# Optimization experiments

Measured on AMD Instinct MI355X. Metric: run time of the kernel, lower is better.

Reference implementation:

```python
import jax, jax.numpy as jnp
import numpy as np

NEG_BIG = 1e30  # matches the 1e+30 masking constant in the original


def setup_inputs() -> dict:
    key = jax.random.key(0)
    ks = jax.random.split(key, 6)
    B, Lc, Lq, D = 8, 512, 64, 256
    return {
        "context": jax.random.normal(ks[0], (B, Lc, D), jnp.float32),
        "question": jax.random.normal(ks[1], (B, Lq, D), jnp.float32),
        "mask": jnp.ones((B, Lq), jnp.int32),
        "att_w": jax.random.normal(ks[2], (3 * D,), jnp.float32) * 0.05,  # Linear(6H=3D -> 1) weight
        "att_b": jnp.zeros((1,), jnp.float32),                            # Linear bias
        "w_in": jax.random.normal(ks[3], (D,), jnp.float32) * 0.05,       # input_linear (no bias)
        "w_mem": jax.random.normal(ks[4], (D,), jnp.float32) * 0.05,      # memory_linear (no bias)
    }


def reference(context, question, mask, att_w, att_b, w_in, w_mem):
    # context: [B,Lc,D], question: [B,Lq,D], mask: [B,Lq] (0/1)
    D = context.shape[-1]
    # Separable (mathematically identical) form of Linear(cat([c, q, c*q])):
    # score[b,i,j] = c_i . w_c + q_j . w_q + sum_d c[b,i,d]*q[b,j,d]*w_p[d] + b
    w_c, w_q, w_p = att_w[:D], att_w[D:2 * D], att_w[2 * D:]
    sc = jnp.einsum('bid,d->bi', context, w_c)                 # [B,Lc]
    sq = jnp.einsum('bjd,d->bj', question, w_q)                # [B,Lq]
    sp = jnp.einsum('bid,bjd->bij', context * w_p, question)   # [B,Lc,Lq]
    attention = sc[:, :, None] + sq[:, None, :] + sp + att_b[0]

    maskf = mask.astype(attention.dtype)
    masked = attention - NEG_BIG * (1.0 - maskf)[:, None, :]   # [B,Lc,Lq]

    ctx1 = jnp.einsum('bid,d->bi', context, w_in)[..., None]   # input_linear:  [B,Lc,1]
    q1 = jnp.einsum('bjd,d->bj', question, w_mem)[..., None]   # memory_linear: [B,Lq,1]

    h_aware_weight = jax.nn.softmax(masked, axis=-1)           # [B,Lc,Lq]
    U = jnp.matmul(h_aware_weight, q1)                         # [B,Lc,1]

    u_aware_weight = jax.nn.softmax(jnp.max(masked, axis=-1), axis=-1)[:, None, :]  # [B,1,Lc]
    H = jnp.matmul(u_aware_weight, ctx1)                       # [B,1,1]

    G = jnp.concatenate([ctx1, U, ctx1 * U, U * H], axis=-1)   # [B,Lc,4]
    return G
```

## Files before the change

kernel.cpp:

```cpp
#include <hip/hip_runtime.h>

#define NB 8
#define LC 512
#define LQ 64
#define DD 256
#define NEG_BIG_F 1e30f

#define TPB 512
#define NWAVE 8
#define RPB 8
#define BPB (LC / RPB)

__device__ __forceinline__ float bcastf(float x, int lane) {
  return __uint_as_float((unsigned)__builtin_amdgcn_readlane((int)__float_as_uint(x), lane));
}

__global__ __launch_bounds__(TPB, 4) void rows_kernel(
    const float* __restrict__ context,
    const float* __restrict__ question,
    const int*   __restrict__ mask,
    const float* __restrict__ att_w,
    const float* __restrict__ att_b,
    const float* __restrict__ w_in,
    const float* __restrict__ w_mem,
    float4* __restrict__ ws4)
{
  __shared__ float4 T[64][64];
  __shared__ float sq_raw[LQ];
  __shared__ float q1_s[LQ];

  const int tid  = threadIdx.x;
  const int w    = tid >> 6;
  const int l    = tid & 63;
  const int b    = blockIdx.x / BPB;
  const int row0 = (blockIdx.x % BPB) * RPB;
  const int i    = row0 + w;

  const float4 wc4 = ((const float4*)att_w)[l];
  const float4 wq4 = ((const float4*)(att_w + DD))[l];
  const float4 wp4 = ((const float4*)(att_w + 2 * DD))[l];
  const float4 wi4 = ((const float4*)w_in)[l];
  const float4 wm4 = ((const float4*)w_mem)[l];
  const float4 c4  = ((const float4*)(context + ((size_t)b * LC + i) * DD))[l];

  float4 v[8];
#pragma unroll
  for (int k = 0; k < 8; ++k)
    v[k] = ((const float4*)(question + ((size_t)b * LQ + (k * 8 + w)) * DD))[l];
#pragma unroll
  for (int k = 0; k < 8; ++k)
    T[l][(k * 8 + w) ^ (l & 7)] = v[k];

  float psq[8], pq1[8];
#pragma unroll
  for (int k = 0; k < 8; ++k) {
    psq[k] = v[k].x*wq4.x + v[k].y*wq4.y + v[k].z*wq4.z + v[k].w*wq4.w;
    pq1[k] = v[k].x*wm4.x + v[k].y*wm4.y + v[k].z*wm4.z + v[k].w*wm4.w;
  }
#pragma unroll
  for (int off = 32; off > 0; off >>= 1) {
#pragma unroll
    for (int k = 0; k < 8; ++k) {
      psq[k] += __shfl_xor(psq[k], off);
      pq1[k] += __shfl_xor(pq1[k], off);
    }
  }
  if (l == 0) {
#pragma unroll
    for (int k = 0; k < 8; ++k) {
      sq_raw[k * 8 + w] = psq[k];
      q1_s[k * 8 + w]   = pq1[k];
    }
  }

  float4 cp;
  cp.x = c4.x*wp4.x; cp.y = c4.y*wp4.y; cp.z = c4.z*wp4.z; cp.w = c4.w*wp4.w;
  float sc = c4.x*wc4.x + c4.y*wc4.y + c4.z*wc4.z + c4.w*wc4.w;
  float c1 = c4.x*wi4.x + c4.y*wi4.y + c4.z*wi4.z + c4.w*wi4.w;
#pragma unroll
  for (int off = 32; off > 0; off >>= 1) {
    sc += __shfl_xor(sc, off);
    c1 += __shfl_xor(c1, off);
  }

  __syncthreads();

  float a0 = 0.f, a1 = 0.f, a2 = 0.f, a3 = 0.f;
#pragma unroll
  for (int c = 0; c < 64; ++c) {
    float4 qv = T[c][l ^ (c & 7)];
    a0 += bcastf(cp.x, c) * qv.x;
    a1 += bcastf(cp.y, c) * qv.y;
    a2 += bcastf(cp.z, c) * qv.z;
    a3 += bcastf(cp.w, c) * qv.w;
  }

  const float mf = (float)mask[b * LQ + l];
  const float vscore = (a0 + a1) + (a2 + a3) + sc + sq_raw[l] + att_b[0]
                       - NEG_BIG_F * (1.0f - mf);
  const float q1_l = q1_s[l];

  float m = vscore;
#pragma unroll
  for (int off = 32; off > 0; off >>= 1) m = fmaxf(m, __shfl_xor(m, off));
  float p  = __expf(vscore - m);
  float ps = p;
  float pu = p * q1_l;
#pragma unroll
  for (int off = 32; off > 0; off >>= 1) {
    ps += __shfl_xor(ps, off);
    pu += __shfl_xor(pu, off);
  }
  if (l == 0)
    ws4[b * LC + i] = make_float4(m, c1, pu / ps, 0.f);
}

__global__ __launch_bounds__(512) void batch_kernel(
    const float4* __restrict__ ws4,
    float4* __restrict__ out4)
{
  const int b  = blockIdx.x;
  const int t  = threadIdx.x;
  const int gi = b * LC + t;
  const float4 v = ws4[gi];
  const float m = v.x, c1 = v.y, U = v.z;

  const int w = t >> 6, l = t & 63;
  __shared__ float rmax[8], rs[8], rc[8];

  float mx = m;
#pragma unroll
  for (int off = 32; off > 0; off >>= 1) mx = fmaxf(mx, __shfl_xor(mx, off));
  if (l == 0) rmax[w] = mx;
  __syncthreads();
  mx = rmax[0];
#pragma unroll
  for (int k = 1; k < 8; ++k) mx = fmaxf(mx, rmax[k]);

  float p  = __expf(m - mx);
  float ps = p;
  float pc = p * c1;
#pragma unroll
  for (int off = 32; off > 0; off >>= 1) {
    ps += __shfl_xor(ps, off);
    pc += __shfl_xor(pc, off);
  }
  if (l == 0) { rs[w] = ps; rc[w] = pc; }
  __syncthreads();
  float S = 0.f, C = 0.f;
#pragma unroll
  for (int k = 0; k < 8; ++k) { S += rs[k]; C += rc[k]; }

  const float H = C / S;
  out4[gi] = make_float4(c1, U, c1 * U, U * H);
}

extern "C" void kernel_launch(void* const* d_in, const int* in_sizes, int n_in,
                              void* d_out, int out_size, void* d_ws, size_t ws_size,
                              hipStream_t stream) {
  const float* context  = (const float*)d_in[0];
  const float* question = (const float*)d_in[1];
  const int*   mask     = (const int*)d_in[2];
  const float* att_w    = (const float*)d_in[3];
  const float* att_b    = (const float*)d_in[4];
  const float* w_in     = (const float*)d_in[5];
  const float* w_mem    = (const float*)d_in[6];
  float4* out4 = (float4*)d_out;
  float4* ws4  = (float4*)d_ws;

  rows_kernel<<<dim3(NB * BPB), dim3(TPB), 0, stream>>>(
      context, question, mask, att_w, att_b, w_in, w_mem, ws4);
  batch_kernel<<<dim3(NB), dim3(512), 0, stream>>>(ws4, out4);
}
```

Before: 77.50 us.

## Fuse batch reduction into rows kernel via last-block atomic counter

Merges the second per-batch kernel into the row kernel. Each block bumps a per-batch atomic counter, and the last block to finish a batch does the cross-row softmax and writes the output. This removes one kernel launch and the gap between the two dependent launches. In exchange it adds a memset of the counters before the launch and atomic/acquire-release synchronization.

```diff
diff --git a/kernel.cpp b/kernel.cpp
--- a/kernel.cpp
+++ b/kernel.cpp
@@ -7,15 +7,16 @@
 #define NEG_BIG_F 1e30f
 
 #define TPB 512
-#define NWAVE 8
 #define RPB 8
 #define BPB (LC / RPB)
+
+#define CNT_OFF_BYTES (128 * 1024)
 
 __device__ __forceinline__ float bcastf(float x, int lane) {
   return __uint_as_float((unsigned)__builtin_amdgcn_readlane((int)__float_as_uint(x), lane));
 }
 
-__global__ __launch_bounds__(TPB, 4) void rows_kernel(
+__global__ __launch_bounds__(TPB, 4) void fused_kernel(
     const float* __restrict__ context,
     const float* __restrict__ question,
     const int*   __restrict__ mask,
@@ -23,11 +24,14 @@
     const float* __restrict__ att_b,
     const float* __restrict__ w_in,
     const float* __restrict__ w_mem,
-    float4* __restrict__ ws4)
+    float4* __restrict__ ws4,
+    unsigned* __restrict__ cnt,
+    float4* __restrict__ out4)
 {
   __shared__ float4 T[64][64];
   __shared__ float sq_raw[LQ];
   __shared__ float q1_s[LQ];
+  __shared__ int   is_last;
 
   const int tid  = threadIdx.x;
   const int w    = tid >> 6;
@@ -113,22 +117,25 @@
   }
   if (l == 0)
     ws4[b * LC + i] = make_float4(m, c1, pu / ps, 0.f);
-}
 
-__global__ __launch_bounds__(512) void batch_kernel(
-    const float4* __restrict__ ws4,
-    float4* __restrict__ out4)
-{
-  const int b  = blockIdx.x;
-  const int t  = threadIdx.x;
+  __syncthreads();
+  if (tid == 0) {
+    unsigned prev = __hip_atomic_fetch_add(&cnt[b], 1u, __ATOMIC_ACQ_REL,
+                                           __HIP_MEMORY_SCOPE_AGENT);
+    is_last = (prev == (unsigned)(BPB - 1));
+  }
+  __syncthreads();
+  if (!is_last) return;
+
+  (void)__hip_atomic_load(&cnt[b], __ATOMIC_ACQUIRE, __HIP_MEMORY_SCOPE_AGENT);
+
+  const int t  = tid;
   const int gi = b * LC + t;
-  const float4 v = ws4[gi];
-  const float m = v.x, c1 = v.y, U = v.z;
+  const float4 vv = ws4[gi];
+  const float mr = vv.x, c1r = vv.y, Ur = vv.z;
 
-  const int w = t >> 6, l = t & 63;
   __shared__ float rmax[8], rs[8], rc[8];
-
-  float mx = m;
+  float mx = mr;
 #pragma unroll
   for (int off = 32; off > 0; off >>= 1) mx = fmaxf(mx, __shfl_xor(mx, off));
   if (l == 0) rmax[w] = mx;
@@ -137,22 +144,22 @@
 #pragma unroll
   for (int k = 1; k < 8; ++k) mx = fmaxf(mx, rmax[k]);
 
-  float p  = __expf(m - mx);
-  float ps = p;
-  float pc = p * c1;
+  float pp = __expf(mr - mx);
+  float pS = pp;
+  float pC = pp * c1r;
 #pragma unroll
   for (int off = 32; off > 0; off >>= 1) {
-    ps += __shfl_xor(ps, off);
-    pc += __shfl_xor(pc, off);
+    pS += __shfl_xor(pS, off);
+    pC += __shfl_xor(pC, off);
   }
-  if (l == 0) { rs[w] = ps; rc[w] = pc; }
+  if (l == 0) { rs[w] = pS; rc[w] = pC; }
   __syncthreads();
   float S = 0.f, C = 0.f;
 #pragma unroll
   for (int k = 0; k < 8; ++k) { S += rs[k]; C += rc[k]; }
 
   const float H = C / S;
-  out4[gi] = make_float4(c1, U, c1 * U, U * H);
+  out4[gi] = make_float4(c1r, Ur, c1r * Ur, Ur * H);
 }
 
 extern "C" void kernel_launch(void* const* d_in, const int* in_sizes, int n_in,
@@ -165,10 +172,11 @@
   const float* att_b    = (const float*)d_in[4];
   const float* w_in     = (const float*)d_in[5];
   const float* w_mem    = (const float*)d_in[6];
-  float4* out4 = (float4*)d_out;
-  float4* ws4  = (float4*)d_ws;
+  float4*   out4 = (float4*)d_out;
+  float4*   ws4  = (float4*)d_ws;
+  unsigned* cnt  = (unsigned*)((char*)d_ws + CNT_OFF_BYTES);
 
-  rows_kernel<<<dim3(NB * BPB), dim3(TPB), 0, stream>>>(
-      context, question, mask, att_w, att_b, w_in, w_mem, ws4);
-  batch_kernel<<<dim3(NB), dim3(512), 0, stream>>>(ws4, out4);
+  hipMemsetAsync(cnt, 0, NB * sizeof(unsigned), stream);
+  fused_kernel<<<dim3(NB * BPB), dim3(TPB), 0, stream>>>(
+      context, question, mask, att_w, att_b, w_in, w_mem, ws4, cnt, out4);
 }
```

New measurement: 88.69 us. +14.4%, slower.
